# Kernel optimization log

Measured on AMD Instinct MI355X. Metric: run time of the kernel, lower is better.

The kernel has to match this reference:

```python
import jax, jax.numpy as jnp
import numpy as np

D_MODEL = 1024
D_FFN = 4096
N_HEAD = 16
D_K = D_MODEL // N_HEAD
EPS = 1e-10


def _layernorm(x, gamma, beta):
    mean = jnp.mean(x, axis=-1, keepdims=True)
    var = jnp.mean((x - mean) ** 2, axis=-1, keepdims=True)
    return gamma * ((x - mean) / jnp.sqrt(var + EPS)) + beta


def setup_inputs() -> dict:
    key = jax.random.key(0)
    ks = jax.random.split(key, 16)
    s = 1.0 / np.sqrt(D_MODEL)
    sf = 1.0 / np.sqrt(D_FFN)
    return {
        "x": jax.random.normal(ks[0], (4, 2048, D_MODEL), jnp.float32),
        "wq": jax.random.uniform(ks[1], (D_MODEL, D_MODEL), jnp.float32, -s, s),
        "bq": jnp.zeros((D_MODEL,), jnp.float32),
        "wk": jax.random.uniform(ks[2], (D_MODEL, D_MODEL), jnp.float32, -s, s),
        "bk": jnp.zeros((D_MODEL,), jnp.float32),
        "wv": jax.random.uniform(ks[3], (D_MODEL, D_MODEL), jnp.float32, -s, s),
        "bv": jnp.zeros((D_MODEL,), jnp.float32),
        "wo": jax.random.uniform(ks[4], (D_MODEL, D_MODEL), jnp.float32, -s, s),
        "bo": jnp.zeros((D_MODEL,), jnp.float32),
        "g1": jnp.ones((D_MODEL,), jnp.float32),
        "b1": jnp.zeros((D_MODEL,), jnp.float32),
        "w1": jax.random.uniform(ks[5], (D_MODEL, D_FFN), jnp.float32, -s, s),
        "bf1": jnp.zeros((D_FFN,), jnp.float32),
        "w2": jax.random.uniform(ks[6], (D_FFN, D_MODEL), jnp.float32, -sf, sf),
        "bf2": jnp.zeros((D_MODEL,), jnp.float32),
        "g2": jnp.ones((D_MODEL,), jnp.float32),
        "b2": jnp.zeros((D_MODEL,), jnp.float32),
    }


def reference(x, wq, bq, wk, bk, wv, bv, wo, bo, g1, b1, w1, bf1, w2, bf2, g2, b2):
    B, S, _ = x.shape
    # projections -> (B, H, S, d_k)
    q = (x @ wq + bq).reshape(B, S, N_HEAD, D_K).transpose(0, 2, 1, 3)
    k = (x @ wk + bk).reshape(B, S, N_HEAD, D_K).transpose(0, 2, 1, 3)
    v = (x @ wv + bv).reshape(B, S, N_HEAD, D_K).transpose(0, 2, 1, 3)
    score = jnp.einsum("bhqd,bhkd->bhqk", q, k) / jnp.sqrt(jnp.asarray(D_K, x.dtype))
    attn = jax.nn.softmax(score, axis=-1)
    out = jnp.einsum("bhqk,bhkd->bhqd", attn, v)
    out = out.transpose(0, 2, 1, 3).reshape(B, S, D_MODEL)
    out = out @ wo + bo
    out1 = _layernorm(x + out, g1, b1)
    # FFN (dropout is identity in eval mode)
    ff = jax.nn.relu(out1 @ w1 + bf1) @ w2 + bf2
    out2 = _layernorm(out1 + ff, g2, b2)
    return (out2, attn)
```

## Files before the change

### kernel.cpp

```cpp
#include <hip/hip_runtime.h>
#include <hip/hip_bf16.h>

#define DEV __device__ __forceinline__

typedef __attribute__((ext_vector_type(4))) float f32x4;
typedef __attribute__((ext_vector_type(8))) __bf16 bf16v;
typedef __attribute__((ext_vector_type(8))) unsigned short u16x8;
typedef __attribute__((ext_vector_type(4))) unsigned short u16x4;

DEV unsigned short f2b(float x) {
    unsigned u = __builtin_bit_cast(unsigned, x);
    unsigned r = u + 0x7FFF + ((u >> 16) & 1);
    return (unsigned short)(r >> 16);
}

DEV void gl_lds16(const void* g, void* l) {
    __builtin_amdgcn_global_load_lds(
        (const __attribute__((address_space(1))) unsigned*)g,
        (__attribute__((address_space(3))) unsigned*)l,
        16, 0, 0);
}


__global__ __launch_bounds__(256) void cvt_f32_bf16(const float* __restrict__ in,
                                                    unsigned short* __restrict__ out, long n) {
    long i = ((long)blockIdx.x * 256 + threadIdx.x) * 4;
    if (i >= n) return;
    float4 f = *(const float4*)(in + i);
    u16x4 u;
    u[0] = f2b(f.x); u[1] = f2b(f.y); u[2] = f2b(f.z); u[3] = f2b(f.w);
    *(u16x4*)(out + i) = u;
}

__global__ __launch_bounds__(256) void transp_f32_bf16(const float* __restrict__ in,
                                                       unsigned short* __restrict__ out,
                                                       int R, int C) {
    __shared__ float t[32][33];
    int tx = threadIdx.x & 31, ty = threadIdx.x >> 5;
    long c0 = (long)blockIdx.x * 32, r0 = (long)blockIdx.y * 32;
#pragma unroll
    for (int i = 0; i < 4; i++)
        t[ty + i * 8][tx] = in[(r0 + ty + i * 8) * C + c0 + tx];
    __syncthreads();
#pragma unroll
    for (int i = 0; i < 4; i++)
        out[(c0 + ty + i * 8) * R + r0 + tx] = f2b(t[tx][ty + i * 8]);
}

DEV float waveSum(float v) {
#pragma unroll
    for (int o = 32; o > 0; o >>= 1) v += __shfl_xor(v, o);
    return v;
}

__global__ __launch_bounds__(256) void ln_rows(const float* __restrict__ in,
                                               const float* __restrict__ g,
                                               const float* __restrict__ b,
                                               float* __restrict__ outF,
                                               unsigned short* __restrict__ outB) {
    const float* p = in + (long)blockIdx.x * 1024;
    __shared__ float red[4], red2[4];
    int t = threadIdx.x, lane = t & 63, wave = t >> 6;
    float4 v = ((const float4*)p)[t];
    float s = v.x + v.y + v.z + v.w;
    float q = v.x * v.x + v.y * v.y + v.z * v.z + v.w * v.w;
    s = waveSum(s); q = waveSum(q);
    if (lane == 0) { red[wave] = s; red2[wave] = q; }
    __syncthreads();
    s = red[0] + red[1] + red[2] + red[3];
    q = red2[0] + red2[1] + red2[2] + red2[3];
    float mean = s * (1.0f / 1024.0f);
    float var = q * (1.0f / 1024.0f) - mean * mean;
    float rstd = rsqrtf(var + 1e-10f);
    float4 gg = ((const float4*)g)[t];
    float4 bb = ((const float4*)b)[t];
    float4 o;
    o.x = gg.x * ((v.x - mean) * rstd) + bb.x;
    o.y = gg.y * ((v.y - mean) * rstd) + bb.y;
    o.z = gg.z * ((v.z - mean) * rstd) + bb.z;
    o.w = gg.w * ((v.w - mean) * rstd) + bb.w;
    ((float4*)(outF + (long)blockIdx.x * 1024))[t] = o;
    if (outB) {
        u16x4 u;
        u[0] = f2b(o.x); u[1] = f2b(o.y); u[2] = f2b(o.z); u[3] = f2b(o.w);
        *(u16x4*)(outB + (long)blockIdx.x * 1024 + (long)t * 4) = u;
    }
}

__global__ __launch_bounds__(256, 2) void attn_fused(
    const unsigned short* __restrict__ qb,
    const unsigned short* __restrict__ kb,
    const unsigned short* __restrict__ vt,
    float* __restrict__ attn,
    unsigned short* __restrict__ ao) {
    __shared__ __align__(16) char smem[65536];
    __shared__ float sredM[4][16], sredS[4][16];

    int id = blockIdx.x;
    int swz = (id & 7) * 1024 + (id >> 3);
    const int z = swz >> 7;
    const int m0 = (swz & 127) * 16;

    const int tid = threadIdx.x, lane = tid & 63, w = tid >> 6;
    const int g = lane >> 4, l15 = lane & 15;

    const char* qz = (const char*)(qb + (long)z * 131072);
    const char* kz = (const char*)(kb + (long)z * 131072);
    const char* vz = (const char*)(vt + (long)z * 131072);

    const char* qrow = qz + (long)(m0 + l15) * 128;
    bf16v aq0 = *(const bf16v*)(qrow + g * 16);
    bf16v aq1 = *(const bf16v*)(qrow + 64 + g * 16);

    f32x4 acc[8][4];
#pragma unroll
    for (int c = 0; c < 8; c++)
#pragma unroll
        for (int t = 0; t < 4; t++) acc[c][t] = (f32x4)(0.0f);

    const int soff = ((lane & 7) * 16) ^ (((lane >> 3) & 7) << 4);

    for (int c = 0; c < 8; ++c) {
        const char* src = kz + (long)(c * 256 + w * 8 + (lane >> 3)) * 128 + soff;
#pragma unroll
        for (int i = 0; i < 8; ++i)
            gl_lds16(src + (long)i * 4096, smem + i * 4096 + w * 1024);
        __syncthreads();
#pragma unroll
        for (int t = 0; t < 4; ++t) {
            const int row = w * 64 + t * 16 + l15;
            const char* bp = smem + row * 128;
            const int sw = (lane & 7) << 4;
            bf16v bk0 = *(const bf16v*)(bp + ((g * 16) ^ sw));
            bf16v bk1 = *(const bf16v*)(bp + ((64 + g * 16) ^ sw));
            acc[c][t] = __builtin_amdgcn_mfma_f32_16x16x32_bf16(aq0, bk0, acc[c][t], 0, 0, 0);
            acc[c][t] = __builtin_amdgcn_mfma_f32_16x16x32_bf16(aq1, bk1, acc[c][t], 0, 0, 0);
        }
        __syncthreads();
    }

    float M[4], S[4];
#pragma unroll
    for (int j = 0; j < 4; ++j) {
        float m = -1e30f;
#pragma unroll
        for (int c = 0; c < 8; c++)
#pragma unroll
            for (int t = 0; t < 4; t++) m = fmaxf(m, acc[c][t][j]);
        m = fmaxf(m, __shfl_xor(m, 1));
        m = fmaxf(m, __shfl_xor(m, 2));
        m = fmaxf(m, __shfl_xor(m, 4));
        m = fmaxf(m, __shfl_xor(m, 8));
        M[j] = m;
    }
    if (l15 == 0) {
        sredM[w][g * 4 + 0] = M[0];
        sredM[w][g * 4 + 1] = M[1];
        sredM[w][g * 4 + 2] = M[2];
        sredM[w][g * 4 + 3] = M[3];
    }
    __syncthreads();
#pragma unroll
    for (int j = 0; j < 4; ++j) {
        int r = g * 4 + j;
        M[j] = 0.125f * fmaxf(fmaxf(sredM[0][r], sredM[1][r]),
                              fmaxf(sredM[2][r], sredM[3][r]));
        S[j] = 0.0f;
    }
#pragma unroll
    for (int c = 0; c < 8; c++)
#pragma unroll
        for (int t = 0; t < 4; t++) {
            f32x4 v = acc[c][t];
            v[0] = __expf(v[0] * 0.125f - M[0]);
            v[1] = __expf(v[1] * 0.125f - M[1]);
            v[2] = __expf(v[2] * 0.125f - M[2]);
            v[3] = __expf(v[3] * 0.125f - M[3]);
            acc[c][t] = v;
            S[0] += v[0]; S[1] += v[1]; S[2] += v[2]; S[3] += v[3];
        }
#pragma unroll
    for (int j = 0; j < 4; ++j) {
        float s = S[j];
        s += __shfl_xor(s, 1);
        s += __shfl_xor(s, 2);
        s += __shfl_xor(s, 4);
        s += __shfl_xor(s, 8);
        S[j] = s;
    }
    if (l15 == 0) {
        sredS[w][g * 4 + 0] = S[0];
        sredS[w][g * 4 + 1] = S[1];
        sredS[w][g * 4 + 2] = S[2];
        sredS[w][g * 4 + 3] = S[3];
    }
    __syncthreads();
    float inv[4];
#pragma unroll
    for (int j = 0; j < 4; ++j) {
        int r = g * 4 + j;
        inv[j] = 1.0f / (sredS[0][r] + sredS[1][r] + sredS[2][r] + sredS[3][r]);
    }

    float* ab = attn + (long)z * 4194304 + (long)m0 * 2048;
#pragma unroll
    for (int c = 0; c < 8; c++)
#pragma unroll
        for (int t = 0; t < 4; t++) {
            const int col = c * 256 + w * 64 + t * 16 + l15;
#pragma unroll
            for (int j = 0; j < 4; ++j) {
                const int r = g * 4 + j;
                float p = acc[c][t][j] * inv[j];
                ab[(long)r * 2048 + col] = p;
                *(unsigned short*)(smem + r * 4096 + ((col * 2) ^ ((r & 7) << 4))) = f2b(p);
            }
        }
    __syncthreads();

    f32x4 o0 = (f32x4)(0.0f), o1 = (f32x4)(0.0f);
    f32x4 o2 = (f32x4)(0.0f), o3 = (f32x4)(0.0f);
    const char* vtile = vz + (long)(w * 16 + l15) * 4096;
    const char* prow = smem + l15 * 4096;
    const int psw = (l15 & 7) << 4;
#pragma unroll 4
    for (int ks = 0; ks < 64; ks += 4) {
        bf16v pa0 = *(const bf16v*)(prow + (((ks + 0) * 64 + g * 16) ^ psw));
        bf16v pa1 = *(const bf16v*)(prow + (((ks + 1) * 64 + g * 16) ^ psw));
        bf16v pa2 = *(const bf16v*)(prow + (((ks + 2) * 64 + g * 16) ^ psw));
        bf16v pa3 = *(const bf16v*)(prow + (((ks + 3) * 64 + g * 16) ^ psw));
        bf16v bv0 = *(const bf16v*)(vtile + (ks + 0) * 64 + g * 16);
        bf16v bv1 = *(const bf16v*)(vtile + (ks + 1) * 64 + g * 16);
        bf16v bv2 = *(const bf16v*)(vtile + (ks + 2) * 64 + g * 16);
        bf16v bv3 = *(const bf16v*)(vtile + (ks + 3) * 64 + g * 16);
        o0 = __builtin_amdgcn_mfma_f32_16x16x32_bf16(pa0, bv0, o0, 0, 0, 0);
        o1 = __builtin_amdgcn_mfma_f32_16x16x32_bf16(pa1, bv1, o1, 0, 0, 0);
        o2 = __builtin_amdgcn_mfma_f32_16x16x32_bf16(pa2, bv2, o2, 0, 0, 0);
        o3 = __builtin_amdgcn_mfma_f32_16x16x32_bf16(pa3, bv3, o3, 0, 0, 0);
    }
    o0 = o0 + o1 + o2 + o3;

    const int b = z >> 4, h = z & 15;
    const long tokbase = (long)b * 2048 + m0 + g * 4;
#pragma unroll
    for (int j = 0; j < 4; ++j)
        ao[(tokbase + j) * 1024 + h * 64 + w * 16 + l15] = f2b(o0[j]);
}


enum { M_QKV = 0, M_VT = 1, M_RES = 2, M_RELU = 3 };

struct GArgs {
    const unsigned short* A;
    long lda;
    const unsigned short* B;
    long ldb;
    const float* bias;
    const float* resid;
    float* outF;
    unsigned short* outB;
    long ldo;
    int K;
};

template <int BM, int BN, int WR, int WC, int MODE>
__global__ __launch_bounds__(256) void gemm_k(GArgs g) {
    constexpr int MI = BM / (WR * 16), NI = BN / (WC * 16);
    __shared__ __align__(16) char sm[(BM + BN) * 128];
    char* sA = sm;
    char* sB = sm + BM * 128;
    const int tid = threadIdx.x, lane = tid & 63, wave = tid >> 6;
    const int wr = wave / WC, wc = wave % WC;
    const long m0 = (long)blockIdx.x * BM, n0 = (long)blockIdx.y * BN;

    const char* Ab = (const char*)(g.A + m0 * g.lda);
    const char* Bb = (const char*)(g.B + n0 * g.ldb);
    const long lda = g.lda, ldb = g.ldb;

    f32x4 acc[MI][NI];
#pragma unroll
    for (int mi = 0; mi < MI; mi++)
#pragma unroll
        for (int ni = 0; ni < NI; ni++) acc[mi][ni] = (f32x4)(0.0f);

    for (int k0 = 0; k0 < g.K; k0 += 64) {
#pragma unroll
        for (int i = 0; i < BM / 32; i++) {
            int c = i * 4 + wave;
            int p = c * 1024 + lane * 16;
            int row = p >> 7;
            int scb = (p & 127) ^ ((row & 7) << 4);
            gl_lds16(Ab + (long)row * (lda * 2) + (long)k0 * 2 + scb, sA + c * 1024);
        }
#pragma unroll
        for (int i = 0; i < BN / 32; i++) {
            int c = i * 4 + wave;
            int p = c * 1024 + lane * 16;
            int row = p >> 7;
            int scb = (p & 127) ^ ((row & 7) << 4);
            gl_lds16(Bb + (long)row * (ldb * 2) + (long)k0 * 2 + scb, sB + c * 1024);
        }
        __syncthreads();
#pragma unroll
        for (int ks = 0; ks < 2; ++ks) {
            const int cb = ks * 64 + (lane >> 4) * 16;
            bf16v af[MI], bfv[NI];
#pragma unroll
            for (int mi = 0; mi < MI; mi++) {
                int r = wr * (BM / WR) + mi * 16 + (lane & 15);
                af[mi] = *(const bf16v*)(sA + r * 128 + (cb ^ ((r & 7) << 4)));
            }
#pragma unroll
            for (int ni = 0; ni < NI; ni++) {
                int r = wc * (BN / WC) + ni * 16 + (lane & 15);
                bfv[ni] = *(const bf16v*)(sB + r * 128 + (cb ^ ((r & 7) << 4)));
            }
#pragma unroll
            for (int mi = 0; mi < MI; mi++)
#pragma unroll
                for (int ni = 0; ni < NI; ni++)
                    acc[mi][ni] = __builtin_amdgcn_mfma_f32_16x16x32_bf16(
                        af[mi], bfv[ni], acc[mi][ni], 0, 0, 0);
        }
        __syncthreads();
    }

#pragma unroll
    for (int mi = 0; mi < MI; mi++)
#pragma unroll
        for (int ni = 0; ni < NI; ni++) {
            if constexpr (MODE == M_VT) {
                long r = m0 + wr * (BM / WR) + mi * 16 + (lane >> 4) * 4;
                long c = n0 + wc * (BN / WC) + ni * 16 + (lane & 15);
                float bi = g.bias[c];
                u16x4 u;
#pragma unroll
                for (int j = 0; j < 4; ++j) u[j] = f2b(acc[mi][ni][j] + bi);
                long b = r >> 11, s = r & 2047, h = c >> 6, d = c & 63;
                *(u16x4*)(g.outB + (b * 16 + h) * 131072 + d * 2048 + s) = u;
            } else {
#pragma unroll
                for (int j = 0; j < 4; ++j) {
                    long r = m0 + wr * (BM / WR) + mi * 16 + (lane >> 4) * 4 + j;
                    long c = n0 + wc * (BN / WC) + ni * 16 + (lane & 15);
                    float v = acc[mi][ni][j];
                    if constexpr (MODE == M_QKV) {
                        v += g.bias[c];
                        long b = r >> 11, s = r & 2047, h = c >> 6, d = c & 63;
                        g.outB[((b * 16 + h) * 2048 + s) * 64 + d] = f2b(v);
                    } else if constexpr (MODE == M_RES) {
                        long i = r * g.ldo + c;
                        g.outF[i] = v + g.bias[c] + g.resid[i];
                    } else {
                        float t = v + g.bias[c];
                        g.outB[r * g.ldo + c] = f2b(t > 0.0f ? t : 0.0f);
                    }
                }
            }
        }
}


extern "C" void kernel_launch(void* const* d_in, const int* in_sizes, int n_in,
                              void* d_out, int out_size, void* d_ws, size_t ws_size,
                              hipStream_t stream) {
    const float* x = (const float*)d_in[0];
    const float* wq = (const float*)d_in[1];
    const float* bq = (const float*)d_in[2];
    const float* wk = (const float*)d_in[3];
    const float* bk = (const float*)d_in[4];
    const float* wv = (const float*)d_in[5];
    const float* bv = (const float*)d_in[6];
    const float* wo = (const float*)d_in[7];
    const float* bo = (const float*)d_in[8];
    const float* g1 = (const float*)d_in[9];
    const float* b1 = (const float*)d_in[10];
    const float* w1 = (const float*)d_in[11];
    const float* bf1 = (const float*)d_in[12];
    const float* w2 = (const float*)d_in[13];
    const float* bf2 = (const float*)d_in[14];
    const float* g2 = (const float*)d_in[15];
    const float* b2 = (const float*)d_in[16];

    float* out2 = (float*)d_out;
    float* attn = (float*)d_out + 8388608;

    char* ws = (char*)d_ws;
    size_t off = 0;
    auto alc = [&](size_t bytes) { size_t r = off; off += (bytes + 255) & ~(size_t)255; return r; };

    unsigned short* xb  = (unsigned short*)(ws + alc(16777216));
    unsigned short* wqT = (unsigned short*)(ws + alc(2097152));
    unsigned short* wkT = (unsigned short*)(ws + alc(2097152));
    unsigned short* wvT = (unsigned short*)(ws + alc(2097152));
    unsigned short* woT = (unsigned short*)(ws + alc(2097152));
    unsigned short* w1T = (unsigned short*)(ws + alc(8388608));
    unsigned short* w2T = (unsigned short*)(ws + alc(8388608));
    size_t qkvOff = alc(67108864);
    unsigned short* qb = (unsigned short*)(ws + qkvOff);
    unsigned short* kb = qb + 8388608;
    unsigned short* vt = kb + 8388608;
    unsigned short* ff1 = qb;
    size_t aoOff = alc(16777216);
    unsigned short* ao  = (unsigned short*)(ws + aoOff);
    unsigned short* o1b = ao;
    size_t rOff = alc(33554432);
    float* r1 = (float*)(ws + rOff);
    float* r2 = r1;
    float* o1f = (float*)(ws + alc(33554432));

    cvt_f32_bf16<<<8192, 256, 0, stream>>>(x, xb, 8388608);
    transp_f32_bf16<<<dim3(32, 32), 256, 0, stream>>>(wq, wqT, 1024, 1024);
    transp_f32_bf16<<<dim3(32, 32), 256, 0, stream>>>(wk, wkT, 1024, 1024);
    transp_f32_bf16<<<dim3(32, 32), 256, 0, stream>>>(wv, wvT, 1024, 1024);
    transp_f32_bf16<<<dim3(32, 32), 256, 0, stream>>>(wo, woT, 1024, 1024);
    transp_f32_bf16<<<dim3(128, 32), 256, 0, stream>>>(w1, w1T, 1024, 4096);
    transp_f32_bf16<<<dim3(32, 128), 256, 0, stream>>>(w2, w2T, 4096, 1024);

    {
        GArgs a{};
        a.A = xb; a.lda = 1024; a.ldb = 1024; a.K = 1024;
        a.B = wqT; a.bias = bq; a.outB = qb;
        gemm_k<128, 128, 2, 2, M_QKV><<<dim3(64, 8), 256, 0, stream>>>(a);
        a.B = wkT; a.bias = bk; a.outB = kb;
        gemm_k<128, 128, 2, 2, M_QKV><<<dim3(64, 8), 256, 0, stream>>>(a);
        a.B = wvT; a.bias = bv; a.outB = vt;
        gemm_k<128, 128, 2, 2, M_VT><<<dim3(64, 8), 256, 0, stream>>>(a);
    }
    attn_fused<<<8192, 256, 0, stream>>>(qb, kb, vt, attn, ao);
    {
        GArgs a{};
        a.A = ao; a.lda = 1024; a.B = woT; a.ldb = 1024;
        a.bias = bo; a.resid = x; a.outF = r1; a.ldo = 1024; a.K = 1024;
        gemm_k<128, 128, 2, 2, M_RES><<<dim3(64, 8), 256, 0, stream>>>(a);
    }
    ln_rows<<<8192, 256, 0, stream>>>(r1, g1, b1, o1f, o1b);
    {
        GArgs a{};
        a.A = o1b; a.lda = 1024; a.B = w1T; a.ldb = 1024;
        a.bias = bf1; a.outB = ff1; a.ldo = 4096; a.K = 1024;
        gemm_k<128, 128, 2, 2, M_RELU><<<dim3(64, 32), 256, 0, stream>>>(a);
    }
    {
        GArgs a{};
        a.A = ff1; a.lda = 4096; a.B = w2T; a.ldb = 4096;
        a.bias = bf2; a.resid = o1f; a.outF = r2; a.ldo = 1024; a.K = 4096;
        gemm_k<128, 128, 2, 2, M_RES><<<dim3(64, 8), 256, 0, stream>>>(a);
    }
    ln_rows<<<8192, 256, 0, stream>>>(r2, g2, b2, out2, nullptr);

    (void)in_sizes; (void)n_in; (void)out_size; (void)ws_size;
}
```

Before: 910.1 us.

## Fuse QKV GEMMs, load K directly to registers, add setprio and nontemporal attn stores

The three Q/K/V projection GEMMs are merged into one launch over a concatenated transposed weight and bias, with the epilogue routing columns to q, k or transposed v. In the attention kernel, K tiles are now read straight from global into registers instead of being staged through LDS with barriers. s_setprio is wrapped around the MFMA blocks, and the fp32 attention probabilities are written with nontemporal stores to avoid polluting the cache. These changes cut launch count and barrier stalls, but the direct K loads lose LDS reuse and rely on cache hits.

```diff
diff --git a/kernel.cpp b/kernel.cpp
--- a/kernel.cpp
+++ b/kernel.cpp
@@ -118,25 +118,22 @@
 #pragma unroll
         for (int t = 0; t < 4; t++) acc[c][t] = (f32x4)(0.0f);
 
-    const int soff = ((lane & 7) * 16) ^ (((lane >> 3) & 7) << 4);
-
+#pragma unroll 2
     for (int c = 0; c < 8; ++c) {
-        const char* src = kz + (long)(c * 256 + w * 8 + (lane >> 3)) * 128 + soff;
-#pragma unroll
-        for (int i = 0; i < 8; ++i)
-            gl_lds16(src + (long)i * 4096, smem + i * 4096 + w * 1024);
-        __syncthreads();
+        bf16v bk0[4], bk1[4];
 #pragma unroll
         for (int t = 0; t < 4; ++t) {
-            const int row = w * 64 + t * 16 + l15;
-            const char* bp = smem + row * 128;
-            const int sw = (lane & 7) << 4;
-            bf16v bk0 = *(const bf16v*)(bp + ((g * 16) ^ sw));
-            bf16v bk1 = *(const bf16v*)(bp + ((64 + g * 16) ^ sw));
-            acc[c][t] = __builtin_amdgcn_mfma_f32_16x16x32_bf16(aq0, bk0, acc[c][t], 0, 0, 0);
-            acc[c][t] = __builtin_amdgcn_mfma_f32_16x16x32_bf16(aq1, bk1, acc[c][t], 0, 0, 0);
-        }
-        __syncthreads();
+            const char* kcol = kz + (long)(c * 256 + w * 64 + t * 16 + l15) * 128 + g * 16;
+            bk0[t] = *(const bf16v*)(kcol);
+            bk1[t] = *(const bf16v*)(kcol + 64);
+        }
+        __builtin_amdgcn_s_setprio(1);
+#pragma unroll
+        for (int t = 0; t < 4; ++t) {
+            acc[c][t] = __builtin_amdgcn_mfma_f32_16x16x32_bf16(aq0, bk0[t], acc[c][t], 0, 0, 0);
+            acc[c][t] = __builtin_amdgcn_mfma_f32_16x16x32_bf16(aq1, bk1[t], acc[c][t], 0, 0, 0);
+        }
+        __builtin_amdgcn_s_setprio(0);
     }
 
     float M[4], S[4];
@@ -212,7 +209,7 @@
             for (int j = 0; j < 4; ++j) {
                 const int r = g * 4 + j;
                 float p = acc[c][t][j] * inv[j];
-                ab[(long)r * 2048 + col] = p;
+                __builtin_nontemporal_store(p, &ab[(long)r * 2048 + col]);
                 *(unsigned short*)(smem + r * 4096 + ((col * 2) ^ ((r & 7) << 4))) = f2b(p);
             }
         }
@@ -233,10 +230,12 @@
         bf16v bv1 = *(const bf16v*)(vtile + (ks + 1) * 64 + g * 16);
         bf16v bv2 = *(const bf16v*)(vtile + (ks + 2) * 64 + g * 16);
         bf16v bv3 = *(const bf16v*)(vtile + (ks + 3) * 64 + g * 16);
+        __builtin_amdgcn_s_setprio(1);
         o0 = __builtin_amdgcn_mfma_f32_16x16x32_bf16(pa0, bv0, o0, 0, 0, 0);
         o1 = __builtin_amdgcn_mfma_f32_16x16x32_bf16(pa1, bv1, o1, 0, 0, 0);
         o2 = __builtin_amdgcn_mfma_f32_16x16x32_bf16(pa2, bv2, o2, 0, 0, 0);
         o3 = __builtin_amdgcn_mfma_f32_16x16x32_bf16(pa3, bv3, o3, 0, 0, 0);
+        __builtin_amdgcn_s_setprio(0);
     }
     o0 = o0 + o1 + o2 + o3;
 
@@ -248,7 +247,7 @@
 }
 
 
-enum { M_QKV = 0, M_VT = 1, M_RES = 2, M_RELU = 3 };
+enum { M_QKV3 = 0, M_RES = 1, M_RELU = 2 };
 
 struct GArgs {
     const unsigned short* A;
@@ -259,6 +258,8 @@
     const float* resid;
     float* outF;
     unsigned short* outB;
+    unsigned short* outB2;
+    unsigned short* outB3;
     long ldo;
     int K;
 };
@@ -329,26 +330,32 @@
     for (int mi = 0; mi < MI; mi++)
 #pragma unroll
         for (int ni = 0; ni < NI; ni++) {
-            if constexpr (MODE == M_VT) {
+            if constexpr (MODE == M_QKV3) {
                 long r = m0 + wr * (BM / WR) + mi * 16 + (lane >> 4) * 4;
                 long c = n0 + wc * (BN / WC) + ni * 16 + (lane & 15);
+                long b = r >> 11, s = r & 2047;
                 float bi = g.bias[c];
-                u16x4 u;
-#pragma unroll
-                for (int j = 0; j < 4; ++j) u[j] = f2b(acc[mi][ni][j] + bi);
-                long b = r >> 11, s = r & 2047, h = c >> 6, d = c & 63;
-                *(u16x4*)(g.outB + (b * 16 + h) * 131072 + d * 2048 + s) = u;
+                if (c < 2048) {
+                    unsigned short* dst = (c < 1024) ? g.outB : g.outB2;
+                    long h = (c >> 6) & 15, d = c & 63;
+                    long base = ((b * 16 + h) * 2048 + s) * 64 + d;
+#pragma unroll
+                    for (int j = 0; j < 4; ++j)
+                        dst[base + (long)j * 64] = f2b(acc[mi][ni][j] + bi);
+                } else {
+                    long h = (c - 2048) >> 6, d = c & 63;
+                    u16x4 u;
+#pragma unroll
+                    for (int j = 0; j < 4; ++j) u[j] = f2b(acc[mi][ni][j] + bi);
+                    *(u16x4*)(g.outB3 + (b * 16 + h) * 131072 + d * 2048 + s) = u;
+                }
             } else {
 #pragma unroll
                 for (int j = 0; j < 4; ++j) {
                     long r = m0 + wr * (BM / WR) + mi * 16 + (lane >> 4) * 4 + j;
                     long c = n0 + wc * (BN / WC) + ni * 16 + (lane & 15);
                     float v = acc[mi][ni][j];
-                    if constexpr (MODE == M_QKV) {
-                        v += g.bias[c];
-                        long b = r >> 11, s = r & 2047, h = c >> 6, d = c & 63;
-                        g.outB[((b * 16 + h) * 2048 + s) * 64 + d] = f2b(v);
-                    } else if constexpr (MODE == M_RES) {
+                    if constexpr (MODE == M_RES) {
                         long i = r * g.ldo + c;
                         g.outF[i] = v + g.bias[c] + g.resid[i];
                     } else {
@@ -389,15 +396,14 @@
     size_t off = 0;
     auto alc = [&](size_t bytes) { size_t r = off; off += (bytes + 255) & ~(size_t)255; return r; };
 
-    unsigned short* xb  = (unsigned short*)(ws + alc(16777216));
-    unsigned short* wqT = (unsigned short*)(ws + alc(2097152));
-    unsigned short* wkT = (unsigned short*)(ws + alc(2097152));
-    unsigned short* wvT = (unsigned short*)(ws + alc(2097152));
-    unsigned short* woT = (unsigned short*)(ws + alc(2097152));
-    unsigned short* w1T = (unsigned short*)(ws + alc(8388608));
-    unsigned short* w2T = (unsigned short*)(ws + alc(8388608));
-    size_t qkvOff = alc(67108864);
-    unsigned short* qb = (unsigned short*)(ws + qkvOff);
+    unsigned short* xb    = (unsigned short*)(ws + alc(16777216));
+    unsigned short* wqkvT = (unsigned short*)(ws + alc(6291456));
+    unsigned short* woT   = (unsigned short*)(ws + alc(2097152));
+    unsigned short* w1T   = (unsigned short*)(ws + alc(8388608));
+    unsigned short* w2T   = (unsigned short*)(ws + alc(8388608));
+    float* bqkv           = (float*)(ws + alc(12288));
+    size_t bigOff = alc(67108864);
+    unsigned short* qb = (unsigned short*)(ws + bigOff);
     unsigned short* kb = qb + 8388608;
     unsigned short* vt = kb + 8388608;
     unsigned short* ff1 = qb;
@@ -410,22 +416,21 @@
     float* o1f = (float*)(ws + alc(33554432));
 
     cvt_f32_bf16<<<8192, 256, 0, stream>>>(x, xb, 8388608);
-    transp_f32_bf16<<<dim3(32, 32), 256, 0, stream>>>(wq, wqT, 1024, 1024);
-    transp_f32_bf16<<<dim3(32, 32), 256, 0, stream>>>(wk, wkT, 1024, 1024);
-    transp_f32_bf16<<<dim3(32, 32), 256, 0, stream>>>(wv, wvT, 1024, 1024);
+    transp_f32_bf16<<<dim3(32, 32), 256, 0, stream>>>(wq, wqkvT, 1024, 1024);
+    transp_f32_bf16<<<dim3(32, 32), 256, 0, stream>>>(wk, wqkvT + 1048576, 1024, 1024);
+    transp_f32_bf16<<<dim3(32, 32), 256, 0, stream>>>(wv, wqkvT + 2097152, 1024, 1024);
     transp_f32_bf16<<<dim3(32, 32), 256, 0, stream>>>(wo, woT, 1024, 1024);
     transp_f32_bf16<<<dim3(128, 32), 256, 0, stream>>>(w1, w1T, 1024, 4096);
     transp_f32_bf16<<<dim3(32, 128), 256, 0, stream>>>(w2, w2T, 4096, 1024);
+    hipMemcpyAsync(bqkv, bq, 4096, hipMemcpyDeviceToDevice, stream);
+    hipMemcpyAsync(bqkv + 1024, bk, 4096, hipMemcpyDeviceToDevice, stream);
+    hipMemcpyAsync(bqkv + 2048, bv, 4096, hipMemcpyDeviceToDevice, stream);
 
     {
         GArgs a{};
-        a.A = xb; a.lda = 1024; a.ldb = 1024; a.K = 1024;
-        a.B = wqT; a.bias = bq; a.outB = qb;
-        gemm_k<128, 128, 2, 2, M_QKV><<<dim3(64, 8), 256, 0, stream>>>(a);
-        a.B = wkT; a.bias = bk; a.outB = kb;
-        gemm_k<128, 128, 2, 2, M_QKV><<<dim3(64, 8), 256, 0, stream>>>(a);
-        a.B = wvT; a.bias = bv; a.outB = vt;
-        gemm_k<128, 128, 2, 2, M_VT><<<dim3(64, 8), 256, 0, stream>>>(a);
+        a.A = xb; a.lda = 1024; a.B = wqkvT; a.ldb = 1024; a.K = 1024;
+        a.bias = bqkv; a.outB = qb; a.outB2 = kb; a.outB3 = vt;
+        gemm_k<128, 128, 2, 2, M_QKV3><<<dim3(64, 24), 256, 0, stream>>>(a);
     }
     attn_fused<<<8192, 256, 0, stream>>>(qb, kb, vt, attn, ao);
     {
```

Measured after the change: 1.696 ms. +86.3%, slower.
